# Kernel optimization log

Measured on AMD Instinct MI355X. Metric: run time of the kernel, lower is better.

The kernel has to match this reference:

```python
import jax, jax.numpy as jnp
import numpy as np

N_NODES = 50000
N_EDGES = 500000
NUM_RADIAL = 6
HIDDEN = 128

def swish(v):
    return v * jax.nn.sigmoid(v)

def setup_inputs() -> dict:
    key = jax.random.key(0)
    ks = jax.random.split(key, 8)
    x = jax.random.randint(ks[0], (N_NODES,), 0, 95, dtype=jnp.int32)
    rbf = jax.random.normal(ks[1], (N_EDGES, NUM_RADIAL), dtype=jnp.float32)
    i = jax.random.randint(ks[2], (N_EDGES,), 0, N_NODES, dtype=jnp.int32)
    j = jax.random.randint(ks[3], (N_EDGES,), 0, N_NODES, dtype=jnp.int32)
    sqrt3 = np.sqrt(3.0).astype(np.float32)
    emb_weight = jax.random.uniform(ks[4], (95, HIDDEN), minval=-sqrt3, maxval=sqrt3, dtype=jnp.float32)
    w_rbf0 = jax.random.normal(ks[5], (HIDDEN, NUM_RADIAL), dtype=jnp.float32) * 0.2
    b_rbf0 = jnp.zeros((HIDDEN,), dtype=jnp.float32)
    w_lin = jax.random.normal(ks[6], (HIDDEN, 3 * HIDDEN), dtype=jnpp.float32) if False else jax.random.normal(ks[6], (HIDDEN, 3 * HIDDEN), dtype=jnp.float32) * 0.05
    b_lin = jnp.zeros((HIDDEN,), dtype=jnp.float32)
    w_rbf1 = jax.random.normal(ks[7], (HIDDEN, NUM_RADIAL), dtype=jnp.float32) * 0.4
    return {"x": x, "rbf": rbf, "i": i, "j": j, "emb_weight": emb_weight,
            "w_rbf0": w_rbf0, "b_rbf0": b_rbf0, "w_lin": w_lin, "b_lin": b_lin,
            "w_rbf1": w_rbf1}

def reference(x, rbf, i, j, emb_weight, w_rbf0, b_rbf0, w_lin, b_lin, w_rbf1):
    # node embedding lookup: [N, H]
    h = emb_weight[x]
    # rbf0 = swish(rbf @ W0^T + b0): [E, H]
    rbf0 = swish(jnp.einsum('er,hr->eh', rbf, w_rbf0) + b_rbf0)
    # gather endpoint embeddings and concat with rbf0: [E, 3H]
    cat = jnp.concatenate([h[i], h[j], rbf0], axis=-1)
    e1 = swish(jnp.einsum('ek,hk->eh', cat, w_lin) + b_lin)
    e2 = jnp.einsum('er,hr->eh', rbf, w_rbf1) * e1
    return (e1, e2)
```

## Files before the change

### kernel.cpp

```cpp
#include <hip/hip_runtime.h>

#define HIDDEN 128
#define NRAD 6
#define NEMB 95
#define PLD 132
#define SLD 136

typedef short bf16x8 __attribute__((ext_vector_type(8)));
typedef float f32x4 __attribute__((ext_vector_type(4)));

__device__ __forceinline__ float fast_rcp(float x) {
    return __builtin_amdgcn_rcpf(x);
}
__device__ __forceinline__ float swishf(float v) {
    return v * fast_rcp(1.0f + __expf(-v));
}
__device__ __forceinline__ short f2bf(float f) {
    union { float f; unsigned u; } c; c.f = f;
    unsigned r = (c.u + 0x7FFFu + ((c.u >> 16) & 1u)) >> 16;
    return (short)(unsigned short)r;
}
__device__ __forceinline__ float bf2f(unsigned short u) {
    union { unsigned u; float f; } c; c.u = ((unsigned)u) << 16; return c.f;
}
__device__ __forceinline__ unsigned pk(float lo, float hi) {
    return __builtin_amdgcn_perm(__float_as_uint(hi), __float_as_uint(lo), 0x07060302u);
}
__device__ __forceinline__ float xlo(unsigned u) {
    union { unsigned u; float f; } c; c.u = u << 16; return c.f;
}
__device__ __forceinline__ float xhi(unsigned u) {
    union { unsigned u; float f; } c; c.u = u & 0xffff0000u; return c.f;
}

__device__ __forceinline__ void barrier_lgkm() {
    asm volatile("s_waitcnt lgkmcnt(0)" ::: "memory");
    __builtin_amdgcn_s_barrier();
}

__global__ void precompute_kernel(const float* __restrict__ emb,
                                  const float* __restrict__ w_lin,
                                  const float* __restrict__ b_lin,
                                  unsigned short* __restrict__ P1,
                                  unsigned short* __restrict__ P2) {
    __shared__ __align__(16) float erow[HIDDEN];
    const int a = blockIdx.x;
    const int h = threadIdx.x;
    erow[h] = emb[a * HIDDEN + h];
    __syncthreads();
    float acc1 = b_lin[h];
    float acc2 = 0.f;
    const float* __restrict__ w1 = w_lin + h * 384;
    const float* __restrict__ w2 = w1 + HIDDEN;
#pragma unroll 8
    for (int k = 0; k < HIDDEN; ++k) {
        acc1 += erow[k] * w1[k];
        acc2 += erow[k] * w2[k];
    }
    P1[a * PLD + h] = (unsigned short)f2bf(acc1);
    P2[a * PLD + h] = (unsigned short)f2bf(acc2);
}

struct RawMD {
    float2 ra, rb, rc;
    int ii, jj;
};

__device__ __forceinline__ RawMD load_raw(int tile, int l15, int n_edges,
                                          const int* __restrict__ iv,
                                          const int* __restrict__ jv,
                                          const float* __restrict__ rbf) {
    int e = tile * 16 + l15;
    int ecl = (e < n_edges) ? e : (n_edges - 1);
    RawMD m;
    const float2* rp = reinterpret_cast<const float2*>(rbf + (size_t)ecl * NRAD);
    m.ra = rp[0];
    m.rb = rp[1];
    m.rc = rp[2];
    m.ii = iv[ecl];
    m.jj = jv[ecl];
    return m;
}

__global__ __launch_bounds__(256, 2)
void edge_mfma_kernel(const int* __restrict__ xv,
                      const float* __restrict__ rbf,
                      const int* __restrict__ iv,
                      const int* __restrict__ jv,
                      const float* __restrict__ w_rbf0,
                      const float* __restrict__ b_rbf0,
                      const float* __restrict__ w_rbf1,
                      const float* __restrict__ w_lin,
                      const unsigned short* __restrict__ P1g,
                      const unsigned short* __restrict__ P2g,
                      float* __restrict__ out_e1,
                      float* __restrict__ out_e2,
                      int n_edges, int tiles_per_block, int n_tiles, int n_rows) {
    __shared__ __align__(16) unsigned short p1s[NEMB * PLD];
    __shared__ __align__(16) unsigned short p2s[NEMB * PLD];
    __shared__ __align__(16) unsigned short stgE1[2][16 * SLD];
    __shared__ __align__(16) unsigned short stgE2[2][16 * SLD];
    __shared__ __align__(16) short fragS[4 * 4 * 16 * 8];

    const int tid = threadIdx.x;

    {
        const unsigned* __restrict__ g1 = reinterpret_cast<const unsigned*>(P1g);
        const unsigned* __restrict__ g2 = reinterpret_cast<const unsigned*>(P2g);
        unsigned* s1 = reinterpret_cast<unsigned*>(p1s);
        unsigned* s2 = reinterpret_cast<unsigned*>(p2s);
        const int n = (n_rows < NEMB ? n_rows : NEMB) * PLD / 2;
        for (int s = tid; s < n; s += 256) { s1[s] = g1[s]; s2[s] = g2[s]; }
    }

    const int wid = tid >> 6;
    const int lane = tid & 63;
    const int l15 = lane & 15;
    const int lg = lane >> 4;

    const int kbase = wid * 32 + lg * 8;
    float w0r[8][6], b0r[8];
#pragma unroll
    for (int j = 0; j < 8; ++j) {
        const float2* wp = reinterpret_cast<const float2*>(w_rbf0 + (kbase + j) * NRAD);
        const float2 a = wp[0], b = wp[1], c = wp[2];
        w0r[j][0] = a.x; w0r[j][1] = a.y;
        w0r[j][2] = b.x; w0r[j][3] = b.y;
        w0r[j][4] = c.x; w0r[j][5] = c.y;
        b0r[j] = b_rbf0[kbase + j];
    }

    bf16x8 w3f[2][4];
    bf16x8 w1f[2];
#pragma unroll
    for (int n2 = 0; n2 < 2; ++n2) {
        const int h = (wid * 2 + n2) * 16 + l15;
        const float* wp = w_lin + h * 384 + 256;
#pragma unroll
        for (int ks = 0; ks < 4; ++ks) {
            const float4* s4 = reinterpret_cast<const float4*>(wp + (ks * 4 + lg) * 8);
            const float4 va = s4[0];
            const float4 vb = s4[1];
            bf16x8 fr;
            fr[0] = f2bf(va.x); fr[1] = f2bf(va.y);
            fr[2] = f2bf(va.z); fr[3] = f2bf(va.w);
            fr[4] = f2bf(vb.x); fr[5] = f2bf(vb.y);
            fr[6] = f2bf(vb.z); fr[7] = f2bf(vb.w);
            w3f[n2][ks] = fr;
        }
        bf16x8 f1;
#pragma unroll
        for (int r = 0; r < NRAD; ++r) f1[r] = f2bf(w_rbf1[h * NRAD + r]);
        f1[6] = 0; f1[7] = 0;
        w1f[n2] = f1;
    }
    __syncthreads();

    const int bt = blockIdx.x * tiles_per_block;
    const int btEnd = min(bt + tiles_per_block, n_tiles);
    if (bt >= btEnd) return;

    const f32x4 zero4 = (f32x4){0.f, 0.f, 0.f, 0.f};

    RawMD curR = load_raw(bt, l15, n_edges, iv, jv, rbf);
    RawMD nxtR = load_raw(bt + 1, l15, n_edges, iv, jv, rbf);
    int cxi = xv[curR.ii];
    int cxj = xv[curR.jj];

    for (int t = bt; t < btEnd; ++t) {
        RawMD n2R = load_raw(t + 2, l15, n_edges, iv, jv, rbf);
        const int gxi = xv[nxtR.ii];
        const int gxj = xv[nxtR.jj];

        float sv[8];
#pragma unroll
        for (int j = 0; j < 8; ++j) {
            float tv = b0r[j]
                     + curR.ra.x * w0r[j][0] + curR.ra.y * w0r[j][1]
                     + curR.rb.x * w0r[j][2] + curR.rb.y * w0r[j][3]
                     + curR.rc.x * w0r[j][4] + curR.rc.y * w0r[j][5];
            sv[j] = swishf(tv);
        }
        {
            uint4 mf;
            mf.x = pk(sv[0], sv[1]); mf.y = pk(sv[2], sv[3]);
            mf.z = pk(sv[4], sv[5]); mf.w = pk(sv[6], sv[7]);
            *reinterpret_cast<uint4*>(&fragS[((wid * 4 + lg) * 16 + l15) * 8]) = mf;
        }

        union { uint4 u; bf16x8 b; } rp4;
        rp4.u = (uint4){0u, 0u, 0u, 0u};
        if (lg == 0) {
            rp4.u.x = pk(curR.ra.x, curR.ra.y);
            rp4.u.y = pk(curR.rb.x, curR.rb.y);
            rp4.u.z = pk(curR.rc.x, curR.rc.y);
        }
        f32x4 acc2[2];
#pragma unroll
        for (int n2 = 0; n2 < 2; ++n2)
            acc2[n2] = __builtin_amdgcn_mfma_f32_16x16x32_bf16(w1f[n2], rp4.b, zero4, 0, 0, 0);

        barrier_lgkm();

        bf16x8 bfrag[4];
#pragma unroll
        for (int ks = 0; ks < 4; ++ks)
            bfrag[ks] = *reinterpret_cast<const bf16x8*>(
                &fragS[((ks * 4 + lg) * 16 + l15) * 8]);

        f32x4 acc[2] = {zero4, zero4};
#pragma unroll
        for (int ks = 0; ks < 4; ++ks)
#pragma unroll
            for (int n2 = 0; n2 < 2; ++n2)
                acc[n2] = __builtin_amdgcn_mfma_f32_16x16x32_bf16(w3f[n2][ks], bfrag[ks], acc[n2], 0, 0, 0);

        if (t != bt) {
            const int tp = t - 1;
            const int b = tp & 1;
            const size_t base = (size_t)tp * 16 * HIDDEN;
#pragma unroll
            for (int s = 0; s < 2; ++s) {
                const int idx = s * 1024 + tid * 4;
                const int e = idx >> 7;
                const int ch = idx & 127;
                const uint2 u1 = *reinterpret_cast<const uint2*>(&stgE1[b][e * SLD + ch]);
                const uint2 u2 = *reinterpret_cast<const uint2*>(&stgE2[b][e * SLD + ch]);
                if (tp * 16 + e < n_edges) {
                    f32x4 v1, v2;
                    v1[0] = xlo(u1.x); v1[1] = xhi(u1.x); v1[2] = xlo(u1.y); v1[3] = xhi(u1.y);
                    v2[0] = xlo(u2.x); v2[1] = xhi(u2.x); v2[2] = xlo(u2.y); v2[3] = xhi(u2.y);
                    *reinterpret_cast<f32x4*>(out_e1 + base + idx) = v1;
                    *reinterpret_cast<f32x4*>(out_e2 + base + idx) = v2;
                }
            }
        }

#pragma unroll
        for (int n2 = 0; n2 < 2; ++n2) {
            const int ch0 = (wid * 2 + n2) * 16 + lg * 4;
            const uint2 u1 = *reinterpret_cast<const uint2*>(&p1s[cxi * PLD + ch0]);
            const uint2 u2 = *reinterpret_cast<const uint2*>(&p2s[cxj * PLD + ch0]);
            float pv[4];
            pv[0] = bf2f((unsigned short)(u1.x & 0xffff)) + bf2f((unsigned short)(u2.x & 0xffff));
            pv[1] = bf2f((unsigned short)(u1.x >> 16))    + bf2f((unsigned short)(u2.x >> 16));
            pv[2] = bf2f((unsigned short)(u1.y & 0xffff)) + bf2f((unsigned short)(u2.y & 0xffff));
            pv[3] = bf2f((unsigned short)(u1.y >> 16))    + bf2f((unsigned short)(u2.y >> 16));
            float e1v[4], e2v[4];
#pragma unroll
            for (int q = 0; q < 4; ++q) {
                const float s = acc[n2][q] + pv[q];
                e1v[q] = swishf(s);
                e2v[q] = acc2[n2][q] * e1v[q];
            }
            const int so = l15 * SLD + ch0;
            *reinterpret_cast<uint2*>(&stgE1[t & 1][so]) =
                make_uint2(pk(e1v[0], e1v[1]), pk(e1v[2], e1v[3]));
            *reinterpret_cast<uint2*>(&stgE2[t & 1][so]) =
                make_uint2(pk(e2v[0], e2v[1]), pk(e2v[2], e2v[3]));
        }
        barrier_lgkm();

        curR = nxtR; nxtR = n2R; cxi = gxi; cxj = gxj;
    }

    {
        const int tp = btEnd - 1;
        const int b = tp & 1;
        const size_t base = (size_t)tp * 16 * HIDDEN;
#pragma unroll
        for (int s = 0; s < 2; ++s) {
            const int idx = s * 1024 + tid * 4;
            const int e = idx >> 7;
            const int ch = idx & 127;
            const uint2 u1 = *reinterpret_cast<const uint2*>(&stgE1[b][e * SLD + ch]);
            const uint2 u2 = *reinterpret_cast<const uint2*>(&stgE2[b][e * SLD + ch]);
            if (tp * 16 + e < n_edges) {
                f32x4 v1, v2;
                v1[0] = xlo(u1.x); v1[1] = xhi(u1.x); v1[2] = xlo(u1.y); v1[3] = xhi(u1.y);
                v2[0] = xlo(u2.x); v2[1] = xhi(u2.x); v2[2] = xlo(u2.y); v2[3] = xhi(u2.y);
                *reinterpret_cast<f32x4*>(out_e1 + base + idx) = v1;
                *reinterpret_cast<f32x4*>(out_e2 + base + idx) = v2;
            }
        }
    }
}

extern "C" void kernel_launch(void* const* d_in, const int* in_sizes, int n_in,
                              void* d_out, int out_size, void* d_ws, size_t ws_size,
                              hipStream_t stream) {
    const int*   xv     = (const int*)  d_in[0];
    const float* rbf    = (const float*)d_in[1];
    const int*   iv     = (const int*)  d_in[2];
    const int*   jv     = (const int*)  d_in[3];
    const float* emb    = (const float*)d_in[4];
    const float* w_rbf0 = (const float*)d_in[5];
    const float* b_rbf0 = (const float*)d_in[6];
    const float* w_lin  = (const float*)d_in[7];
    const float* b_lin  = (const float*)d_in[8];
    const float* w_rbf1 = (const float*)d_in[9];

    const int n_edges = in_sizes[2];
    const int n_emb_rows = in_sizes[4] / HIDDEN;

    unsigned short* P1 = (unsigned short*)d_ws;
    unsigned short* P2 = P1 + (size_t)NEMB * PLD;

    float* out_e1 = (float*)d_out;
    float* out_e2 = out_e1 + (size_t)n_edges * HIDDEN;

    precompute_kernel<<<n_emb_rows, HIDDEN, 0, stream>>>(emb, w_lin, b_lin, P1, P2);

    const int n_tiles = (n_edges + 15) / 16;
    const int grid = 512;
    const int tpb = (n_tiles + grid - 1) / grid;
    edge_mfma_kernel<<<grid, 256, 0, stream>>>(xv, rbf, iv, jv,
                                               w_rbf0, b_rbf0, w_rbf1, w_lin,
                                               P1, P2, out_e1, out_e2,
                                               n_edges, tpb, n_tiles, n_emb_rows);
}
```

Before: 173.6 us.

## Process 32-edge tiles with per-wave output staging and interleaved P1/P2 table

Each loop iteration now handles two 16-edge subtiles (32 edges), so the MFMA and rbf work of both subtiles sits between fewer block barriers. Output staging becomes per-wave, with each wave writing out its own 32 channels, which removes the barrier that guarded the shared staging buffer. The P1/P2 precomputed tables are packed into one 32-bit pair array, and w_rbf1 fragments move from registers to LDS. This adds more registers and LDS reads per iteration, and occupancy may drop.

New measurement: 158.9 us. 8.5% less time.

```diff
diff --git a/kernel.cpp b/kernel.cpp
--- a/kernel.cpp
+++ b/kernel.cpp
@@ -3,18 +3,12 @@
 #define HIDDEN 128
 #define NRAD 6
 #define NEMB 95
-#define PLD 132
-#define SLD 136
 
 typedef short bf16x8 __attribute__((ext_vector_type(8)));
 typedef float f32x4 __attribute__((ext_vector_type(4)));
 
-__device__ __forceinline__ float fast_rcp(float x) {
-    return __builtin_amdgcn_rcpf(x);
-}
-__device__ __forceinline__ float swishf(float v) {
-    return v * fast_rcp(1.0f + __expf(-v));
-}
+__device__ __forceinline__ float fast_rcp(float x) { return __builtin_amdgcn_rcpf(x); }
+__device__ __forceinline__ float swishf(float v) { return v * fast_rcp(1.0f + __expf(-v)); }
 __device__ __forceinline__ short f2bf(float f) {
     union { float f; unsigned u; } c; c.f = f;
     unsigned r = (c.u + 0x7FFFu + ((c.u >> 16) & 1u)) >> 16;
@@ -32,33 +26,35 @@
 __device__ __forceinline__ float xhi(unsigned u) {
     union { unsigned u; float f; } c; c.u = u & 0xffff0000u; return c.f;
 }
-
 __device__ __forceinline__ void barrier_lgkm() {
     asm volatile("s_waitcnt lgkmcnt(0)" ::: "memory");
     __builtin_amdgcn_s_barrier();
 }
+__device__ __forceinline__ void wait_lgkm() {
+    asm volatile("s_waitcnt lgkmcnt(0)" ::: "memory");
+}
 
 __global__ void precompute_kernel(const float* __restrict__ emb,
                                   const float* __restrict__ w_lin,
                                   const float* __restrict__ b_lin,
-                                  unsigned short* __restrict__ P1,
-                                  unsigned short* __restrict__ P2) {
+                                  unsigned* __restrict__ pPair) {
     __shared__ __align__(16) float erow[HIDDEN];
     const int a = blockIdx.x;
     const int h = threadIdx.x;
     erow[h] = emb[a * HIDDEN + h];
     __syncthreads();
-    float acc1 = b_lin[h];
-    float acc2 = 0.f;
+    float a1 = b_lin[h];
+    float a2 = 0.f;
     const float* __restrict__ w1 = w_lin + h * 384;
     const float* __restrict__ w2 = w1 + HIDDEN;
 #pragma unroll 8
     for (int k = 0; k < HIDDEN; ++k) {
-        acc1 += erow[k] * w1[k];
-        acc2 += erow[k] * w2[k];
-    }
-    P1[a * PLD + h] = (unsigned short)f2bf(acc1);
-    P2[a * PLD + h] = (unsigned short)f2bf(acc2);
+        a1 += erow[k] * w1[k];
+        a2 += erow[k] * w2[k];
+    }
+    const unsigned lo = (unsigned)(unsigned short)f2bf(a1);
+    const unsigned hi = ((unsigned)(unsigned short)f2bf(a2)) << 16;
+    pPair[a * HIDDEN + h] = hi | lo;
 }
 
 struct RawMD {
@@ -66,11 +62,11 @@
     int ii, jj;
 };
 
-__device__ __forceinline__ RawMD load_raw(int tile, int l15, int n_edges,
+__device__ __forceinline__ RawMD load_raw(int st, int l15, int n_edges,
                                           const int* __restrict__ iv,
                                           const int* __restrict__ jv,
                                           const float* __restrict__ rbf) {
-    int e = tile * 16 + l15;
+    int e = st * 16 + l15;
     int ecl = (e < n_edges) ? e : (n_edges - 1);
     RawMD m;
     const float2* rp = reinterpret_cast<const float2*>(rbf + (size_t)ecl * NRAD);
@@ -91,26 +87,27 @@
                       const float* __restrict__ b_rbf0,
                       const float* __restrict__ w_rbf1,
                       const float* __restrict__ w_lin,
-                      const unsigned short* __restrict__ P1g,
-                      const unsigned short* __restrict__ P2g,
+                      const unsigned* __restrict__ pPairG,
                       float* __restrict__ out_e1,
                       float* __restrict__ out_e2,
-                      int n_edges, int tiles_per_block, int n_tiles, int n_rows) {
-    __shared__ __align__(16) unsigned short p1s[NEMB * PLD];
-    __shared__ __align__(16) unsigned short p2s[NEMB * PLD];
-    __shared__ __align__(16) unsigned short stgE1[2][16 * SLD];
-    __shared__ __align__(16) unsigned short stgE2[2][16 * SLD];
-    __shared__ __align__(16) short fragS[4 * 4 * 16 * 8];
+                      int n_edges, int tiles_per_block, int nt32, int n_rows) {
+    __shared__ unsigned pps[NEMB * HIDDEN];
+    __shared__ __align__(16) short fragS[2][16 * 132];
+    __shared__ __align__(8) unsigned short stg[4][2][32 * 36];
+    __shared__ __align__(16) short w1a[HIDDEN * 8];
 
     const int tid = threadIdx.x;
 
     {
-        const unsigned* __restrict__ g1 = reinterpret_cast<const unsigned*>(P1g);
-        const unsigned* __restrict__ g2 = reinterpret_cast<const unsigned*>(P2g);
-        unsigned* s1 = reinterpret_cast<unsigned*>(p1s);
-        unsigned* s2 = reinterpret_cast<unsigned*>(p2s);
-        const int n = (n_rows < NEMB ? n_rows : NEMB) * PLD / 2;
-        for (int s = tid; s < n; s += 256) { s1[s] = g1[s]; s2[s] = g2[s]; }
+        const int n = (n_rows < NEMB ? n_rows : NEMB) * HIDDEN;
+        for (int s = tid; s < n; s += 256) pps[s] = pPairG[s];
+    }
+    if (tid < HIDDEN) {
+        bf16x8 f1;
+#pragma unroll
+        for (int r = 0; r < NRAD; ++r) f1[r] = f2bf(w_rbf1[tid * NRAD + r]);
+        f1[6] = 0; f1[7] = 0;
+        *reinterpret_cast<bf16x8*>(&w1a[tid * 8]) = f1;
     }
 
     const int wid = tid >> 6;
@@ -131,7 +128,6 @@
     }
 
     bf16x8 w3f[2][4];
-    bf16x8 w1f[2];
 #pragma unroll
     for (int n2 = 0; n2 < 2; ++n2) {
         const int h = (wid * 2 + n2) * 16 + l15;
@@ -148,139 +144,177 @@
             fr[6] = f2bf(vb.z); fr[7] = f2bf(vb.w);
             w3f[n2][ks] = fr;
         }
-        bf16x8 f1;
-#pragma unroll
-        for (int r = 0; r < NRAD; ++r) f1[r] = f2bf(w_rbf1[h * NRAD + r]);
-        f1[6] = 0; f1[7] = 0;
-        w1f[n2] = f1;
     }
     __syncthreads();
 
     const int bt = blockIdx.x * tiles_per_block;
-    const int btEnd = min(bt + tiles_per_block, n_tiles);
+    const int btEnd = min(bt + tiles_per_block, nt32);
     if (bt >= btEnd) return;
 
     const f32x4 zero4 = (f32x4){0.f, 0.f, 0.f, 0.f};
 
-    RawMD curR = load_raw(bt, l15, n_edges, iv, jv, rbf);
-    RawMD nxtR = load_raw(bt + 1, l15, n_edges, iv, jv, rbf);
-    int cxi = xv[curR.ii];
-    int cxj = xv[curR.jj];
+    RawMD c0 = load_raw(2 * bt,     l15, n_edges, iv, jv, rbf);
+    RawMD c1 = load_raw(2 * bt + 1, l15, n_edges, iv, jv, rbf);
+    RawMD x0 = load_raw(2 * bt + 2, l15, n_edges, iv, jv, rbf);
+    RawMD x1 = load_raw(2 * bt + 3, l15, n_edges, iv, jv, rbf);
+    int c0i = xv[c0.ii], c0j = xv[c0.jj];
+    int c1i = xv[c1.ii], c1j = xv[c1.jj];
 
     for (int t = bt; t < btEnd; ++t) {
-        RawMD n2R = load_raw(t + 2, l15, n_edges, iv, jv, rbf);
-        const int gxi = xv[nxtR.ii];
-        const int gxj = xv[nxtR.jj];
-
-        float sv[8];
-#pragma unroll
-        for (int j = 0; j < 8; ++j) {
-            float tv = b0r[j]
-                     + curR.ra.x * w0r[j][0] + curR.ra.y * w0r[j][1]
-                     + curR.rb.x * w0r[j][2] + curR.rb.y * w0r[j][3]
-                     + curR.rc.x * w0r[j][4] + curR.rc.y * w0r[j][5];
-            sv[j] = swishf(tv);
-        }
+        RawMD p0 = load_raw(2 * (t + 2),     l15, n_edges, iv, jv, rbf);
+        RawMD p1 = load_raw(2 * (t + 2) + 1, l15, n_edges, iv, jv, rbf);
+        const int g0i = xv[x0.ii], g0j = xv[x0.jj];
+        const int g1i = xv[x1.ii], g1j = xv[x1.jj];
+
         {
+            float sv[8];
+#pragma unroll
+            for (int j = 0; j < 8; ++j) {
+                float tv = b0r[j]
+                         + c0.ra.x * w0r[j][0] + c0.ra.y * w0r[j][1]
+                         + c0.rb.x * w0r[j][2] + c0.rb.y * w0r[j][3]
+                         + c0.rc.x * w0r[j][4] + c0.rc.y * w0r[j][5];
+                sv[j] = swishf(tv);
+            }
             uint4 mf;
             mf.x = pk(sv[0], sv[1]); mf.y = pk(sv[2], sv[3]);
             mf.z = pk(sv[4], sv[5]); mf.w = pk(sv[6], sv[7]);
-            *reinterpret_cast<uint4*>(&fragS[((wid * 4 + lg) * 16 + l15) * 8]) = mf;
-        }
-
-        union { uint4 u; bf16x8 b; } rp4;
-        rp4.u = (uint4){0u, 0u, 0u, 0u};
+            *reinterpret_cast<uint4*>(&fragS[0][(wid * 4 + lg) * 132 + l15 * 8]) = mf;
+        }
+        {
+            float sv[8];
+#pragma unroll
+            for (int j = 0; j < 8; ++j) {
+                float tv = b0r[j]
+                         + c1.ra.x * w0r[j][0] + c1.ra.y * w0r[j][1]
+                         + c1.rb.x * w0r[j][2] + c1.rb.y * w0r[j][3]
+                         + c1.rc.x * w0r[j][4] + c1.rc.y * w0r[j][5];
+                sv[j] = swishf(tv);
+            }
+            uint4 mf;
+            mf.x = pk(sv[0], sv[1]); mf.y = pk(sv[2], sv[3]);
+            mf.z = pk(sv[4], sv[5]); mf.w = pk(sv[6], sv[7]);
+            *reinterpret_cast<uint4*>(&fragS[1][(wid * 4 + lg) * 132 + l15 * 8]) = mf;
+        }
+
+        union { uint4 u; bf16x8 b; } rp0, rp1;
+        rp0.u = (uint4){0u, 0u, 0u, 0u};
+        rp1.u = (uint4){0u, 0u, 0u, 0u};
         if (lg == 0) {
-            rp4.u.x = pk(curR.ra.x, curR.ra.y);
-            rp4.u.y = pk(curR.rb.x, curR.rb.y);
-            rp4.u.z = pk(curR.rc.x, curR.rc.y);
-        }
-        f32x4 acc2[2];
-#pragma unroll
-        for (int n2 = 0; n2 < 2; ++n2)
-            acc2[n2] = __builtin_amdgcn_mfma_f32_16x16x32_bf16(w1f[n2], rp4.b, zero4, 0, 0, 0);
+            rp0.u.x = pk(c0.ra.x, c0.ra.y);
+            rp0.u.y = pk(c0.rb.x, c0.rb.y);
+            rp0.u.z = pk(c0.rc.x, c0.rc.y);
+            rp1.u.x = pk(c1.ra.x, c1.ra.y);
+            rp1.u.y = pk(c1.rb.x, c1.rb.y);
+            rp1.u.z = pk(c1.rc.x, c1.rc.y);
+        }
+        f32x4 acc2[2][2];
+#pragma unroll
+        for (int n2 = 0; n2 < 2; ++n2) {
+            const bf16x8 aw = *reinterpret_cast<const bf16x8*>(
+                &w1a[((wid * 2 + n2) * 16 + l15) * 8]);
+            acc2[0][n2] = __builtin_amdgcn_mfma_f32_16x16x32_bf16(aw, rp0.b, zero4, 0, 0, 0);
+            acc2[1][n2] = __builtin_amdgcn_mfma_f32_16x16x32_bf16(aw, rp1.b, zero4, 0, 0, 0);
+        }
 
         barrier_lgkm();
 
-        bf16x8 bfrag[4];
-#pragma unroll
-        for (int ks = 0; ks < 4; ++ks)
-            bfrag[ks] = *reinterpret_cast<const bf16x8*>(
-                &fragS[((ks * 4 + lg) * 16 + l15) * 8]);
-
-        f32x4 acc[2] = {zero4, zero4};
-#pragma unroll
-        for (int ks = 0; ks < 4; ++ks)
-#pragma unroll
-            for (int n2 = 0; n2 < 2; ++n2)
-                acc[n2] = __builtin_amdgcn_mfma_f32_16x16x32_bf16(w3f[n2][ks], bfrag[ks], acc[n2], 0, 0, 0);
+        f32x4 acc[2][2];
+#pragma unroll
+        for (int u = 0; u < 2; ++u) {
+            bf16x8 bf[4];
+#pragma unroll
+            for (int ks = 0; ks < 4; ++ks)
+                bf[ks] = *reinterpret_cast<const bf16x8*>(
+                    &fragS[u][(ks * 4 + lg) * 132 + l15 * 8]);
+#pragma unroll
+            for (int n2 = 0; n2 < 2; ++n2) acc[u][n2] = zero4;
+#pragma unroll
+            for (int ks = 0; ks < 4; ++ks)
+#pragma unroll
+                for (int n2 = 0; n2 < 2; ++n2)
+                    acc[u][n2] = __builtin_amdgcn_mfma_f32_16x16x32_bf16(
+                        w3f[n2][ks], bf[ks], acc[u][n2], 0, 0, 0);
+        }
+
+        barrier_lgkm();
 
         if (t != bt) {
             const int tp = t - 1;
-            const int b = tp & 1;
-            const size_t base = (size_t)tp * 16 * HIDDEN;
-#pragma unroll
-            for (int s = 0; s < 2; ++s) {
-                const int idx = s * 1024 + tid * 4;
-                const int e = idx >> 7;
-                const int ch = idx & 127;
-                const uint2 u1 = *reinterpret_cast<const uint2*>(&stgE1[b][e * SLD + ch]);
-                const uint2 u2 = *reinterpret_cast<const uint2*>(&stgE2[b][e * SLD + ch]);
-                if (tp * 16 + e < n_edges) {
-                    f32x4 v1, v2;
-                    v1[0] = xlo(u1.x); v1[1] = xhi(u1.x); v1[2] = xlo(u1.y); v1[3] = xhi(u1.y);
-                    v2[0] = xlo(u2.x); v2[1] = xhi(u2.x); v2[2] = xlo(u2.y); v2[3] = xhi(u2.y);
-                    *reinterpret_cast<f32x4*>(out_e1 + base + idx) = v1;
-                    *reinterpret_cast<f32x4*>(out_e2 + base + idx) = v2;
+#pragma unroll
+            for (int arr = 0; arr < 2; ++arr) {
+                float* __restrict__ ob = arr ? out_e2 : out_e1;
+#pragma unroll
+                for (int s = 0; s < 4; ++s) {
+                    const int e = 8 * s + (lane >> 3);
+                    const uint2 u2v = *reinterpret_cast<const uint2*>(
+                        &stg[wid][arr][e * 36 + (lane & 7) * 4]);
+                    const int eg = tp * 32 + e;
+                    if (eg < n_edges) {
+                        f32x4 v;
+                        v[0] = xlo(u2v.x); v[1] = xhi(u2v.x);
+                        v[2] = xlo(u2v.y); v[3] = xhi(u2v.y);
+                        *reinterpret_cast<f32x4*>(
+                            ob + (size_t)eg * HIDDEN + wid * 32 + (lane & 7) * 4) = v;
+                    }
                 }
             }
         }
-
-#pragma unroll
-        for (int n2 = 0; n2 < 2; ++n2) {
-            const int ch0 = (wid * 2 + n2) * 16 + lg * 4;
-            const uint2 u1 = *reinterpret_cast<const uint2*>(&p1s[cxi * PLD + ch0]);
-            const uint2 u2 = *reinterpret_cast<const uint2*>(&p2s[cxj * PLD + ch0]);
-            float pv[4];
-            pv[0] = bf2f((unsigned short)(u1.x & 0xffff)) + bf2f((unsigned short)(u2.x & 0xffff));
-            pv[1] = bf2f((unsigned short)(u1.x >> 16))    + bf2f((unsigned short)(u2.x >> 16));
-            pv[2] = bf2f((unsigned short)(u1.y & 0xffff)) + bf2f((unsigned short)(u2.y & 0xffff));
-            pv[3] = bf2f((unsigned short)(u1.y >> 16))    + bf2f((unsigned short)(u2.y >> 16));
-            float e1v[4], e2v[4];
-#pragma unroll
-            for (int q = 0; q < 4; ++q) {
-                const float s = acc[n2][q] + pv[q];
-                e1v[q] = swishf(s);
-                e2v[q] = acc2[n2][q] * e1v[q];
-            }
-            const int so = l15 * SLD + ch0;
-            *reinterpret_cast<uint2*>(&stgE1[t & 1][so]) =
-                make_uint2(pk(e1v[0], e1v[1]), pk(e1v[2], e1v[3]));
-            *reinterpret_cast<uint2*>(&stgE2[t & 1][so]) =
-                make_uint2(pk(e2v[0], e2v[1]), pk(e2v[2], e2v[3]));
-        }
-        barrier_lgkm();
-
-        curR = nxtR; nxtR = n2R; cxi = gxi; cxj = gxj;
-    }
-
+        wait_lgkm();
+
+#pragma unroll
+        for (int u = 0; u < 2; ++u) {
+            const int xi = u ? c1i : c0i;
+            const int xj = u ? c1j : c0j;
+            const int row = u * 16 + l15;
+#pragma unroll
+            for (int n2 = 0; n2 < 2; ++n2) {
+                const int ch0 = wid * 32 + n2 * 16 + lg * 4;
+                const uint4 r1 = *reinterpret_cast<const uint4*>(&pps[xi * HIDDEN + ch0]);
+                const uint4 r2 = *reinterpret_cast<const uint4*>(&pps[xj * HIDDEN + ch0]);
+                float pv[4];
+                pv[0] = bf2f((unsigned short)(r1.x & 0xffff)) + bf2f((unsigned short)(r2.x >> 16));
+                pv[1] = bf2f((unsigned short)(r1.y & 0xffff)) + bf2f((unsigned short)(r2.y >> 16));
+                pv[2] = bf2f((unsigned short)(r1.z & 0xffff)) + bf2f((unsigned short)(r2.z >> 16));
+                pv[3] = bf2f((unsigned short)(r1.w & 0xffff)) + bf2f((unsigned short)(r2.w >> 16));
+                float e1v[4], e2v[4];
+#pragma unroll
+                for (int q = 0; q < 4; ++q) {
+                    const float s = acc[u][n2][q] + pv[q];
+                    e1v[q] = swishf(s);
+                    e2v[q] = acc2[u][n2][q] * e1v[q];
+                }
+                const int so = row * 36 + n2 * 16 + lg * 4;
+                *reinterpret_cast<uint2*>(&stg[wid][0][so]) =
+                    make_uint2(pk(e1v[0], e1v[1]), pk(e1v[2], e1v[3]));
+                *reinterpret_cast<uint2*>(&stg[wid][1][so]) =
+                    make_uint2(pk(e2v[0], e2v[1]), pk(e2v[2], e2v[3]));
+            }
+        }
+
+        c0 = x0; c1 = x1; x0 = p0; x1 = p1;
+        c0i = g0i; c0j = g0j; c1i = g1i; c1j = g1j;
+    }
+
+    wait_lgkm();
     {
         const int tp = btEnd - 1;
-        const int b = tp & 1;
-        const size_t base = (size_t)tp * 16 * HIDDEN;
-#pragma unroll
-        for (int s = 0; s < 2; ++s) {
-            const int idx = s * 1024 + tid * 4;
-            const int e = idx >> 7;
-            const int ch = idx & 127;
-            const uint2 u1 = *reinterpret_cast<const uint2*>(&stgE1[b][e * SLD + ch]);
-            const uint2 u2 = *reinterpret_cast<const uint2*>(&stgE2[b][e * SLD + ch]);
-            if (tp * 16 + e < n_edges) {
-                f32x4 v1, v2;
-                v1[0] = xlo(u1.x); v1[1] = xhi(u1.x); v1[2] = xlo(u1.y); v1[3] = xhi(u1.y);
-                v2[0] = xlo(u2.x); v2[1] = xhi(u2.x); v2[2] = xlo(u2.y); v2[3] = xhi(u2.y);
-                *reinterpret_cast<f32x4*>(out_e1 + base + idx) = v1;
-                *reinterpret_cast<f32x4*>(out_e2 + base + idx) = v2;
+#pragma unroll
+        for (int arr = 0; arr < 2; ++arr) {
+            float* __restrict__ ob = arr ? out_e2 : out_e1;
+#pragma unroll
+            for (int s = 0; s < 4; ++s) {
+                const int e = 8 * s + (lane >> 3);
+                const uint2 u2v = *reinterpret_cast<const uint2*>(
+                    &stg[wid][arr][e * 36 + (lane & 7) * 4]);
+                const int eg = tp * 32 + e;
+                if (eg < n_edges) {
+                    f32x4 v;
+                    v[0] = xlo(u2v.x); v[1] = xhi(u2v.x);
+                    v[2] = xlo(u2v.y); v[3] = xhi(u2v.y);
+                    *reinterpret_cast<f32x4*>(
+                        ob + (size_t)eg * HIDDEN + wid * 32 + (lane & 7) * 4) = v;
+                }
             }
         }
     }
@@ -303,19 +337,18 @@
     const int n_edges = in_sizes[2];
     const int n_emb_rows = in_sizes[4] / HIDDEN;
 
-    unsigned short* P1 = (unsigned short*)d_ws;
-    unsigned short* P2 = P1 + (size_t)NEMB * PLD;
+    unsigned* pPair = (unsigned*)d_ws;
 
     float* out_e1 = (float*)d_out;
     float* out_e2 = out_e1 + (size_t)n_edges * HIDDEN;
 
-    precompute_kernel<<<n_emb_rows, HIDDEN, 0, stream>>>(emb, w_lin, b_lin, P1, P2);
-
-    const int n_tiles = (n_edges + 15) / 16;
+    precompute_kernel<<<n_emb_rows, HIDDEN, 0, stream>>>(emb, w_lin, b_lin, pPair);
+
+    const int nt32 = (n_edges + 31) / 32;
     const int grid = 512;
-    const int tpb = (n_tiles + grid - 1) / grid;
+    const int tpb = (nt32 + grid - 1) / grid;
     edge_mfma_kernel<<<grid, 256, 0, stream>>>(xv, rbf, iv, jv,
                                                w_rbf0, b_rbf0, w_rbf1, w_lin,
-                                               P1, P2, out_e1, out_e2,
-                                               n_edges, tpb, n_tiles, n_emb_rows);
-}
+                                               pPair, out_e1, out_e2,
+                                               n_edges, tpb, nt32, n_emb_rows);
+}
```
